# Optimization experiments

Measured on AMD Instinct MI355X. Metric: run time of the kernel, lower is better.

## Reference

```python
import jax, jax.numpy as jnp
import numpy as np

BLOCK_H = 1
BLOCK_W = 1
EPS = 1e-6


def setup_inputs() -> dict:
    key = jax.random.key(0)
    ks = jax.random.split(key, 8)
    B, L, D = 2, 4096, 1024
    NBF, DK = 16, 64  # nb_features, d_k (d_model // n_heads)
    ws = 1.0 / np.sqrt(D)  # nn.Linear-like init scale
    return {
        "q": jax.random.normal(ks[0], (B, L, D), jnp.float32),
        "k": jax.random.normal(ks[1], (B, L, D), jnp.float32),
        "v": jax.random.normal(ks[2], (B, L, D), jnp.float32),
        "w_q": jax.random.normal(ks[3], (D, D), jnp.float32) * ws,
        "w_k": jax.random.normal(ks[4], (D, D), jnp.float32) * ws,
        "w_v": jax.random.normal(ks[5], (D, D), jnp.float32) * ws,
        "w_o": jax.random.normal(ks[6], (D, D), jnp.float32) * ws,
        "omega": jax.random.normal(ks[7], (NBF, DK), jnp.float32) / np.sqrt(DK),
    }


def reference(q, k, v, w_q, w_k, w_v, w_o, omega):
    B, Lq, D = q.shape
    Lk = k.shape[1]
    NBF, DK = omega.shape
    H = D // DK

    # projections (torch nn.Linear: x @ W.T), split into heads
    qh = (q @ w_q.T).reshape(B, Lq, H, DK)
    kh = (k @ w_k.T).reshape(B, Lk, H, DK)
    vh = (v @ w_v.T).reshape(B, Lk, H, DK)

    qp = jnp.exp(-0.5 * jnp.square(jnp.einsum('blhd,fd->blhf', qh, omega)))
    kp = jnp.exp(-0.5 * jnp.square(jnp.einsum('blhd,fd->blhf', kh, omega)))
    qp = qp / (qp.sum(-1, keepdims=True) + EPS)
    kp = kp / (kp.sum(-1, keepdims=True) + EPS)

    # causal prefix sums over key positions
    K_cum = jnp.cumsum(kp, axis=1)                                    # [B,Lk,H,F]
    KV_cum = jnp.cumsum(kp[..., None] * vh[..., None, :], axis=1)     # [B,Lk,H,F,DK]

    # blockwise causal key index per query position
    q_idx = jnp.arange(Lq)
    key_idx = jnp.clip((q_idx // BLOCK_H + 1) * BLOCK_W - 1, 0, Lk - 1)
    K_sel = K_cum[:, key_idx]      # [B,Lq,H,F]
    KV_sel = KV_cum[:, key_idx]    # [B,Lq,H,F,DK]

    numerator = jnp.einsum('blhf,blhfd->blhd', qp, KV_sel)
    denominator = jnp.sum(qp * K_sel, axis=-1, keepdims=True)
    out = (numerator / (denominator + EPS)).reshape(B, Lq, D)
    return out @ w_o.T
```

## Files before the change

### kernel.cpp

```cpp
#include <hip/hip_runtime.h>

#define L_SEQ   4096
#define BATCH   2
#define DMODEL  1024
#define HEADS   16
#define DKH     64
#define NBF     16
#define CHUNK   64
#define NCHUNK  64
#define NCHAIN  32
#define STATE_SZ 1040
#define EPSF    1e-6f

typedef __attribute__((ext_vector_type(8))) __bf16 bf16x8;
typedef __attribute__((ext_vector_type(4))) float  floatx4;

__device__ __forceinline__ unsigned short f2bf(float x) {
  unsigned u = __builtin_bit_cast(unsigned, x);
  u += 0x7fffu + ((u >> 16) & 1u);
  return (unsigned short)(u >> 16);
}
__device__ __forceinline__ float bf2f(unsigned short u) {
  return __builtin_bit_cast(float, ((unsigned)u) << 16);
}

#define GLOAD16(gp, lp) \
  __builtin_amdgcn_global_load_lds((const __attribute__((address_space(1))) void*)(gp), \
                                   (__attribute__((address_space(3))) void*)(lp), 16, 0, 0)
#define WAIT_V4L0()  asm volatile("s_waitcnt vmcnt(4) lgkmcnt(0)" ::: "memory")
#define WAIT_V0L0()  asm volatile("s_waitcnt vmcnt(0) lgkmcnt(0)" ::: "memory")
#define SBAR()       __builtin_amdgcn_s_barrier()
#define SCHED0()     __builtin_amdgcn_sched_barrier(0)

__global__ __launch_bounds__(256) void prep(const float* __restrict__ wv, const float* __restrict__ wo,
                                            const float* __restrict__ wq, const float* __restrict__ wk,
                                            const float* __restrict__ omega,
                                            unsigned short* __restrict__ wvb, unsigned short* __restrict__ wob,
                                            unsigned short* __restrict__ wtq, unsigned short* __restrict__ wtk) {
  __shared__ float ws[64 * 64];
  __shared__ float oms[NBF * 64];
  const int blk = blockIdx.x;
  const int tid = threadIdx.x;
  if (blk < 2048) {
    const float* in = (blk < 1024) ? wv : wo;
    unsigned short* out = (blk < 1024) ? wvb : wob;
    int i = (blk & 1023) * 256 + tid;
    float4 v4 = ((const float4*)in)[i];
    ushort4 o;
    o.x = f2bf(v4.x); o.y = f2bf(v4.y); o.z = f2bf(v4.z); o.w = f2bf(v4.w);
    ((ushort4*)out)[i] = o;
    return;
  }
  const int local = blk - 2048;
  const int z = local >> 8;
  const int h = (local & 255) >> 4;
  const int s = local & 15;
  const float* w = z ? wk : wq;
  unsigned short* wt = z ? wtk : wtq;
  for (int i = tid; i < 64 * 64; i += 256) {
    int r = i >> 6, c = i & 63;
    ws[i] = w[(size_t)(h * 64 + r) * DMODEL + s * 64 + c];
  }
  for (int i = tid; i < NBF * 64; i += 256) oms[i] = omega[i];
  __syncthreads();
  for (int j = tid; j < NBF * 64; j += 256) {
    int f = j >> 6, c = j & 63;
    float acc = 0.f;
#pragma unroll
    for (int d = 0; d < 64; ++d) acc += oms[f * 64 + d] * ws[d * 64 + c];
    wt[(size_t)(h * NBF + f) * DMODEL + s * 64 + c] = f2bf(acc);
  }
}

__global__ __launch_bounds__(256) void proj_all(const float* __restrict__ q, const float* __restrict__ k,
                                                const float* __restrict__ v,
                                                const unsigned short* __restrict__ wtq,
                                                const unsigned short* __restrict__ wtk,
                                                const unsigned short* __restrict__ wvb,
                                                float* __restrict__ qp_t, float* __restrict__ kp_t,
                                                unsigned short* __restrict__ vh) {
  constexpr int K = DMODEL, NT = K / 32;
  __shared__ unsigned short As[2][128 * 32];
  __shared__ unsigned short Bs[2][128 * 32];
  const int tid  = threadIdx.x;
  const int wave = tid >> 6, lane = tid & 63;

  const int bid = blockIdx.x;
  const int id = (bid & 7) * 96 + (bid >> 3);
  int op, mt, nt;
  const float* A;
  const unsigned short* Bt;
  if (id < 256) {
    op = id >> 7;
    const int local = id & 127;
    nt = (local & 1) << 7;
    mt = (local >> 1) << 7;
    A  = op ? k : q;
    Bt = op ? wtk : wtq;
  } else {
    op = 2;
    const int local = id - 256;
    nt = (local & 7) << 7;
    mt = (local >> 3) << 7;
    A  = v;
    Bt = wvb;
  }

  const int wm = (wave >> 1) << 6, wn = (wave & 1) << 6;
  const int r16 = lane & 15, kg = lane >> 4;

  floatx4 acc[4][4];
#pragma unroll
  for (int m = 0; m < 4; ++m)
#pragma unroll
    for (int n = 0; n < 4; ++n) acc[m][n] = floatx4{0.f, 0.f, 0.f, 0.f};

  const int ar0  = tid >> 3;
  const int acol = (tid & 7) << 2;
  const float* aG = A + (size_t)(mt + ar0) * K + acol;
  const int ldrow = wave * 16 + (lane >> 2);
  const int ldcol = (lane & 3) << 3;
  const unsigned short* bG = Bt + (size_t)(nt + ldrow) * K + ldcol;

  float4 rA0[4], rA1[4];

  auto loadA = [&](float4* r, int kt) {
#pragma unroll
    for (int j = 0; j < 4; ++j) r[j] = *(const float4*)(aG + (size_t)32 * j * K + kt);
  };
  auto stageB = [&](int buf, int kt) {
    char* bL = (char*)Bs[buf] + wave * 1024;
    GLOAD16(bG + kt, bL);
    GLOAD16(bG + (size_t)64 * K + kt, bL + 4096);
  };
  auto writeA = [&](int buf, const float4* r) {
#pragma unroll
    for (int j = 0; j < 4; ++j) {
      ushort4 u;
      u.x = f2bf(r[j].x); u.y = f2bf(r[j].y); u.z = f2bf(r[j].z); u.w = f2bf(r[j].w);
      *(ushort4*)&As[buf][(ar0 + 32 * j) * 32 + acol] = u;
    }
  };
  auto mfmaStep = [&](int buf) {
    bf16x8 af[4], bfr[4];
#pragma unroll
    for (int m = 0; m < 4; ++m)
      af[m] = *(const bf16x8*)&As[buf][(wm + m * 16 + r16) * 32 + kg * 8];
#pragma unroll
    for (int n = 0; n < 4; ++n)
      bfr[n] = *(const bf16x8*)&Bs[buf][(wn + n * 16 + r16) * 32 + kg * 8];
#pragma unroll
    for (int m = 0; m < 4; ++m)
#pragma unroll
      for (int n = 0; n < 4; ++n)
        acc[m][n] = __builtin_amdgcn_mfma_f32_16x16x32_bf16(af[m], bfr[n], acc[m][n], 0, 0, 0);
  };

  loadA(rA0, 0);
  stageB(0, 0);
  SCHED0();
  writeA(0, rA0);
  loadA(rA1, 32);
  WAIT_V4L0();
  SCHED0();
  SBAR();

  for (int t = 0; t < NT; t += 2) {
    if (t + 1 < NT) stageB(1, (t + 1) * 32);
    SCHED0();
    if (t + 1 < NT) writeA(1, rA1);
    if (t + 2 < NT) loadA(rA0, (t + 2) * 32);
    mfmaStep(0);
    WAIT_V4L0();
    SCHED0();
    SBAR();
    if (t + 2 < NT) stageB(0, (t + 2) * 32);
    SCHED0();
    if (t + 2 < NT) writeA(0, rA0);
    if (t + 3 < NT) loadA(rA1, (t + 3) * 32);
    mfmaStep(1);
    WAIT_V4L0();
    SCHED0();
    SBAR();
  }

  if (op < 2) {
    float* xp_t = op ? kp_t : qp_t;
    const int hbase = (nt + wn) >> 4;
#pragma unroll
    for (int m = 0; m < 4; ++m) {
#pragma unroll
      for (int n = 0; n < 4; ++n) {
        const int hglob = hbase + n;
#pragma unroll
        for (int r = 0; r < 4; ++r) {
          float x = acc[m][n][r];
          float p = __expf(-0.5f * x * x);
          float s = p;
          s += __shfl_xor(s, 1);
          s += __shfl_xor(s, 2);
          s += __shfl_xor(s, 4);
          s += __shfl_xor(s, 8);
          float o = p / (s + EPSF);
          const int row = mt + wm + m * 16 + kg * 4 + r;
          const int b = row >> 12, l = row & 4095;
          xp_t[(((size_t)(b * HEADS + hglob)) * L_SEQ + l) * NBF + r16] = o;
        }
      }
    }
  } else {
#pragma unroll
    for (int m = 0; m < 4; ++m) {
      const int row0 = mt + wm + m * 16 + kg * 4;
#pragma unroll
      for (int n = 0; n < 4; ++n) {
        const int col = nt + wn + n * 16 + r16;
#pragma unroll
        for (int r = 0; r < 4; ++r)
          vh[(size_t)(row0 + r) * DMODEL + col] = f2bf(acc[m][n][r]);
      }
    }
  }
}

__global__ __launch_bounds__(256) void gemm_o(const unsigned short* __restrict__ A,
                                              const unsigned short* __restrict__ Bt,
                                              float* __restrict__ C) {
  constexpr int K = DMODEL, NT = K / 32;
  __shared__ unsigned short As[2][128 * 32];
  __shared__ unsigned short Bs[2][128 * 32];
  const int tid  = threadIdx.x;
  const int wave = tid >> 6, lane = tid & 63;
  const int bid = blockIdx.x;
  const int id = (bid & 7) * 64 + (bid >> 3);
  const int nt = (id & 7) << 7, mt = (id >> 3) << 7;
  const int wm = (wave >> 1) << 6, wn = (wave & 1) << 6;
  const int r16 = lane & 15, kg = lane >> 4;

  floatx4 acc[4][4];
#pragma unroll
  for (int m = 0; m < 4; ++m)
#pragma unroll
    for (int n = 0; n < 4; ++n) acc[m][n] = floatx4{0.f, 0.f, 0.f, 0.f};

  const int ldrow = wave * 16 + (lane >> 2);
  const int ldcol = (lane & 3) << 3;
  const unsigned short* aG = A  + (size_t)(mt + ldrow) * K + ldcol;
  const unsigned short* bG = Bt + (size_t)(nt + ldrow) * K + ldcol;

  auto stage = [&](int buf, int kt) {
    char* aL = (char*)As[buf] + wave * 1024;
    char* bL = (char*)Bs[buf] + wave * 1024;
    GLOAD16(aG + kt, aL);
    GLOAD16(aG + (size_t)64 * K + kt, aL + 4096);
    GLOAD16(bG + kt, bL);
    GLOAD16(bG + (size_t)64 * K + kt, bL + 4096);
  };

  stage(0, 0);
  WAIT_V0L0();
  SCHED0();
  SBAR();
  for (int t = 0; t < NT; ++t) {
    if (t + 1 < NT) stage((t + 1) & 1, (t + 1) * 32);
    const int buf = t & 1;
    bf16x8 af[4], bfr[4];
#pragma unroll
    for (int m = 0; m < 4; ++m)
      af[m] = *(const bf16x8*)&As[buf][(wm + m * 16 + r16) * 32 + kg * 8];
#pragma unroll
    for (int n = 0; n < 4; ++n)
      bfr[n] = *(const bf16x8*)&Bs[buf][(wn + n * 16 + r16) * 32 + kg * 8];
#pragma unroll
    for (int m = 0; m < 4; ++m)
#pragma unroll
      for (int n = 0; n < 4; ++n)
        acc[m][n] = __builtin_amdgcn_mfma_f32_16x16x32_bf16(af[m], bfr[n], acc[m][n], 0, 0, 0);
    WAIT_V0L0();
    SCHED0();
    SBAR();
  }

#pragma unroll
  for (int m = 0; m < 4; ++m) {
    const int row0 = mt + wm + m * 16 + kg * 4;
#pragma unroll
    for (int n = 0; n < 4; ++n) {
      const int col = nt + wn + n * 16 + r16;
#pragma unroll
      for (int r = 0; r < 4; ++r)
        C[(size_t)(row0 + r) * DMODEL + col] = acc[m][n][r];
    }
  }
}

__global__ __launch_bounds__(64) void scan_chunk_sum(const float* __restrict__ kp_t,
                                                     const unsigned short* __restrict__ vh,
                                                     float* __restrict__ Sws) {
  const int c = blockIdx.x & (NCHUNK - 1);
  const int chain = blockIdx.x >> 6;
  const int b = chain >> 4, h = chain & 15;
  const int d = threadIdx.x;
  __shared__ float kp_s[CHUNK * NBF];
  const float* kpB = kp_t + ((size_t)chain * L_SEQ + c * CHUNK) * NBF;
  for (int i = 0; i < 16; ++i) kp_s[d + i * 64] = kpB[d + i * 64];
  __syncthreads();
  float S[NBF];
#pragma unroll
  for (int f = 0; f < NBF; ++f) S[f] = 0.f;
  const unsigned short* vB = vh + ((size_t)(b * L_SEQ + c * CHUNK)) * DMODEL + h * DKH + d;
  for (int l = 0; l < CHUNK; ++l) {
    float vv = bf2f(vB[(size_t)l * DMODEL]);
#pragma unroll
    for (int f = 0; f < NBF; ++f) S[f] += kp_s[l * NBF + f] * vv;
  }
  float* out = Sws + ((size_t)chain * NCHUNK + c) * STATE_SZ;
#pragma unroll
  for (int f = 0; f < NBF; ++f) out[f * 64 + d] = S[f];
  if (d < NBF) {
    float ks = 0.f;
    for (int l = 0; l < CHUNK; ++l) ks += kp_s[l * NBF + d];
    out[1024 + d] = ks;
  }
}

__global__ __launch_bounds__(64) void scan_chunks(float* __restrict__ Sws) {
  const int chain = blockIdx.x;
  const int e = blockIdx.y * 64 + threadIdx.x;
  if (e >= STATE_SZ) return;
  float acc = 0.f;
  float* p = Sws + (size_t)chain * NCHUNK * STATE_SZ + e;
  for (int c = 0; c < NCHUNK; ++c) {
    float v = p[(size_t)c * STATE_SZ];
    p[(size_t)c * STATE_SZ] = acc;
    acc += v;
  }
}

__global__ __launch_bounds__(64) void scan_apply(const float* __restrict__ qp_t,
                                                 const float* __restrict__ kp_t,
                                                 const unsigned short* __restrict__ vh,
                                                 const float* __restrict__ Sws,
                                                 unsigned short* __restrict__ attn) {
  const int c = blockIdx.x & (NCHUNK - 1);
  const int chain = blockIdx.x >> 6;
  const int b = chain >> 4, h = chain & 15;
  const int d = threadIdx.x;
  __shared__ float kp_s[CHUNK * NBF];
  __shared__ float qp_s[CHUNK * NBF];
  {
    const float* kpB = kp_t + ((size_t)chain * L_SEQ + c * CHUNK) * NBF;
    const float* qpB = qp_t + ((size_t)chain * L_SEQ + c * CHUNK) * NBF;
    for (int i = 0; i < 16; ++i) {
      kp_s[d + i * 64] = kpB[d + i * 64];
      qp_s[d + i * 64] = qpB[d + i * 64];
    }
  }
  __syncthreads();
  const float* st = Sws + ((size_t)chain * NCHUNK + c) * STATE_SZ;
  float S[NBF], kc[NBF];
#pragma unroll
  for (int f = 0; f < NBF; ++f) S[f] = st[f * 64 + d];
#pragma unroll
  for (int f = 0; f < NBF; ++f) kc[f] = st[1024 + f];
  const unsigned short* vB = vh + ((size_t)(b * L_SEQ + c * CHUNK)) * DMODEL + h * DKH + d;
  unsigned short* oB = attn + ((size_t)(b * L_SEQ + c * CHUNK)) * DMODEL + h * DKH + d;
  for (int l = 0; l < CHUNK; ++l) {
    float vv = bf2f(vB[(size_t)l * DMODEL]);
    float num = 0.f, den = 0.f;
#pragma unroll
    for (int f = 0; f < NBF; ++f) {
      float kpf = kp_s[l * NBF + f];
      S[f]  += kpf * vv;
      kc[f] += kpf;
      float qpf = qp_s[l * NBF + f];
      num += qpf * S[f];
      den += qpf * kc[f];
    }
    oB[(size_t)l * DMODEL] = f2bf(num / (den + EPSF));
  }
}

extern "C" void kernel_launch(void* const* d_in, const int* in_sizes, int n_in,
                              void* d_out, int out_size, void* d_ws, size_t ws_size,
                              hipStream_t stream) {
  const float* q   = (const float*)d_in[0];
  const float* k   = (const float*)d_in[1];
  const float* v   = (const float*)d_in[2];
  const float* w_q = (const float*)d_in[3];
  const float* w_k = (const float*)d_in[4];
  const float* w_v = (const float*)d_in[5];
  const float* w_o = (const float*)d_in[6];
  const float* omega = (const float*)d_in[7];
  float* out = (float*)d_out;

  constexpr size_t NQ = (size_t)BATCH * L_SEQ * DMODEL;
  constexpr size_t NW = (size_t)DMODEL * DMODEL;
  constexpr size_t NWT = (size_t)HEADS * NBF * DMODEL;
  constexpr size_t NP = (size_t)BATCH * HEADS * L_SEQ * NBF;
  constexpr size_t NS = (size_t)NCHAIN * NCHUNK * STATE_SZ;

  char* ws = (char*)d_ws;
  size_t off = 0;
  auto alc = [&](size_t bytes) { void* p = ws + off; off += (bytes + 255) & ~(size_t)255; return p; };
  unsigned short* wvb = (unsigned short*)alc(NW * 2);
  unsigned short* wob = (unsigned short*)alc(NW * 2);
  unsigned short* wtq = (unsigned short*)alc(NWT * 2);
  unsigned short* wtk = (unsigned short*)alc(NWT * 2);
  unsigned short* vh  = (unsigned short*)alc(NQ * 2);
  unsigned short* attn = (unsigned short*)alc(NQ * 2);
  float* qp  = (float*)alc(NP * 4);
  float* kp  = (float*)alc(NP * 4);
  float* Sws = (float*)alc(NS * 4);

  prep<<<2560, 256, 0, stream>>>(w_v, w_o, w_q, w_k, omega, wvb, wob, wtq, wtk);
  proj_all<<<768, 256, 0, stream>>>(q, k, v, wtq, wtk, wvb, qp, kp, vh);

  scan_chunk_sum<<<NCHAIN * NCHUNK, 64, 0, stream>>>(kp, vh, Sws);
  scan_chunks<<<dim3(NCHAIN, (STATE_SZ + 63) / 64), 64, 0, stream>>>(Sws);
  scan_apply<<<NCHAIN * NCHUNK, 64, 0, stream>>>(qp, kp, vh, Sws, attn);

  gemm_o<<<512, 256, 0, stream>>>(attn, wob, out);
}
```

Before: 169.6 us.

## Swizzle LDS tiles, stage fp32 A via direct loads, drop double buffering

Both GEMM kernels switch to single-buffered LDS tiles with XOR-swizzled column placement, aiming to reduce LDS bank conflicts on the fragment reads. In proj_all the fp32 activations are now copied straight into LDS with global_load_lds and converted to bf16 at fragment-read time, removing the register staging and the convert-then-store path. The hand-tuned double-buffered pipeline with explicit waitcnt and barriers is replaced by a simple load, __syncthreads, compute, __syncthreads loop. This gives up overlap of global loads with MFMA work, which may expose memory latency.

```diff
diff --git a/kernel.cpp b/kernel.cpp
--- a/kernel.cpp
+++ b/kernel.cpp
@@ -27,10 +27,6 @@
 #define GLOAD16(gp, lp) \
   __builtin_amdgcn_global_load_lds((const __attribute__((address_space(1))) void*)(gp), \
                                    (__attribute__((address_space(3))) void*)(lp), 16, 0, 0)
-#define WAIT_V4L0()  asm volatile("s_waitcnt vmcnt(4) lgkmcnt(0)" ::: "memory")
-#define WAIT_V0L0()  asm volatile("s_waitcnt vmcnt(0) lgkmcnt(0)" ::: "memory")
-#define SBAR()       __builtin_amdgcn_s_barrier()
-#define SCHED0()     __builtin_amdgcn_sched_barrier(0)
 
 __global__ __launch_bounds__(256) void prep(const float* __restrict__ wv, const float* __restrict__ wo,
                                             const float* __restrict__ wq, const float* __restrict__ wk,
@@ -79,9 +75,11 @@
                                                 const unsigned short* __restrict__ wvb,
                                                 float* __restrict__ qp_t, float* __restrict__ kp_t,
                                                 unsigned short* __restrict__ vh) {
-  constexpr int K = DMODEL, NT = K / 32;
-  __shared__ unsigned short As[2][128 * 32];
-  __shared__ unsigned short Bs[2][128 * 32];
+  constexpr int K = DMODEL;
+  __shared__ char smem[24576];
+  float* As = (float*)smem;
+  unsigned short* Bs = (unsigned short*)(smem + 16384);
+
   const int tid  = threadIdx.x;
   const int wave = tid >> 6, lane = tid & 63;
 
@@ -115,73 +113,46 @@
 #pragma unroll
     for (int n = 0; n < 4; ++n) acc[m][n] = floatx4{0.f, 0.f, 0.f, 0.f};
 
-  const int ar0  = tid >> 3;
-  const int acol = (tid & 7) << 2;
-  const float* aG = A + (size_t)(mt + ar0) * K + acol;
-  const int ldrow = wave * 16 + (lane >> 2);
-  const int ldcol = (lane & 3) << 3;
-  const unsigned short* bG = Bt + (size_t)(nt + ldrow) * K + ldcol;
-
-  float4 rA0[4], rA1[4];
-
-  auto loadA = [&](float4* r, int kt) {
-#pragma unroll
-    for (int j = 0; j < 4; ++j) r[j] = *(const float4*)(aG + (size_t)32 * j * K + kt);
-  };
-  auto stageB = [&](int buf, int kt) {
-    char* bL = (char*)Bs[buf] + wave * 1024;
-    GLOAD16(bG + kt, bL);
-    GLOAD16(bG + (size_t)64 * K + kt, bL + 4096);
-  };
-  auto writeA = [&](int buf, const float4* r) {
-#pragma unroll
-    for (int j = 0; j < 4; ++j) {
-      ushort4 u;
-      u.x = f2bf(r[j].x); u.y = f2bf(r[j].y); u.z = f2bf(r[j].z); u.w = f2bf(r[j].w);
-      *(ushort4*)&As[buf][(ar0 + 32 * j) * 32 + acol] = u;
-    }
-  };
-  auto mfmaStep = [&](int buf) {
+  const int arow = wave * 32 + (lane >> 3);
+  const int acolsw = ((lane & 7) ^ (lane >> 3)) << 2;
+  const float* aG = A + (size_t)(mt + arow) * K + acolsw;
+  const int brow = wave * 16 + (lane >> 2);
+  const int bcolsw = (((lane & 3) ^ ((lane >> 3) & 3)) << 3);
+  const unsigned short* bG = Bt + (size_t)(nt + brow) * K + bcolsw;
+
+  for (int kt = 0; kt < K; kt += 32) {
+#pragma unroll
+    for (int j = 0; j < 4; ++j)
+      GLOAD16(aG + (size_t)(8 * j) * K + kt, smem + wave * 4096 + j * 1024);
+    GLOAD16(bG + kt, (char*)Bs + wave * 1024);
+    GLOAD16(bG + (size_t)64 * K + kt, (char*)Bs + 4096 + wave * 1024);
+    __syncthreads();
+
     bf16x8 af[4], bfr[4];
 #pragma unroll
-    for (int m = 0; m < 4; ++m)
-      af[m] = *(const bf16x8*)&As[buf][(wm + m * 16 + r16) * 32 + kg * 8];
-#pragma unroll
-    for (int n = 0; n < 4; ++n)
-      bfr[n] = *(const bf16x8*)&Bs[buf][(wn + n * 16 + r16) * 32 + kg * 8];
+    for (int m = 0; m < 4; ++m) {
+      const int row = wm + m * 16 + r16;
+      const int sA = (kg << 1) ^ (r16 & 7);
+      floatx4 lo = *(const floatx4*)(smem + row * 128 + sA * 16);
+      floatx4 hi = *(const floatx4*)(smem + row * 128 + (sA ^ 1) * 16);
+#pragma unroll
+      for (int t2 = 0; t2 < 4; ++t2) {
+        af[m][t2]     = (__bf16)lo[t2];
+        af[m][4 + t2] = (__bf16)hi[t2];
+      }
+    }
+#pragma unroll
+    for (int n = 0; n < 4; ++n) {
+      const int row = wn + n * 16 + r16;
+      const int sB = kg ^ ((r16 >> 1) & 3);
+      bfr[n] = *(const bf16x8*)((char*)Bs + row * 64 + sB * 16);
+    }
 #pragma unroll
     for (int m = 0; m < 4; ++m)
 #pragma unroll
       for (int n = 0; n < 4; ++n)
         acc[m][n] = __builtin_amdgcn_mfma_f32_16x16x32_bf16(af[m], bfr[n], acc[m][n], 0, 0, 0);
-  };
-
-  loadA(rA0, 0);
-  stageB(0, 0);
-  SCHED0();
-  writeA(0, rA0);
-  loadA(rA1, 32);
-  WAIT_V4L0();
-  SCHED0();
-  SBAR();
-
-  for (int t = 0; t < NT; t += 2) {
-    if (t + 1 < NT) stageB(1, (t + 1) * 32);
-    SCHED0();
-    if (t + 1 < NT) writeA(1, rA1);
-    if (t + 2 < NT) loadA(rA0, (t + 2) * 32);
-    mfmaStep(0);
-    WAIT_V4L0();
-    SCHED0();
-    SBAR();
-    if (t + 2 < NT) stageB(0, (t + 2) * 32);
-    SCHED0();
-    if (t + 2 < NT) writeA(0, rA0);
-    if (t + 3 < NT) loadA(rA1, (t + 3) * 32);
-    mfmaStep(1);
-    WAIT_V4L0();
-    SCHED0();
-    SBAR();
+    __syncthreads();
   }
 
   if (op < 2) {
@@ -226,9 +197,9 @@
 __global__ __launch_bounds__(256) void gemm_o(const unsigned short* __restrict__ A,
                                               const unsigned short* __restrict__ Bt,
                                               float* __restrict__ C) {
-  constexpr int K = DMODEL, NT = K / 32;
-  __shared__ unsigned short As[2][128 * 32];
-  __shared__ unsigned short Bs[2][128 * 32];
+  constexpr int K = DMODEL;
+  __shared__ unsigned short As[128 * 32];
+  __shared__ unsigned short Bs[128 * 32];
   const int tid  = threadIdx.x;
   const int wave = tid >> 6, lane = tid & 63;
   const int bid = blockIdx.x;
@@ -244,41 +215,36 @@
     for (int n = 0; n < 4; ++n) acc[m][n] = floatx4{0.f, 0.f, 0.f, 0.f};
 
   const int ldrow = wave * 16 + (lane >> 2);
-  const int ldcol = (lane & 3) << 3;
-  const unsigned short* aG = A  + (size_t)(mt + ldrow) * K + ldcol;
-  const unsigned short* bG = Bt + (size_t)(nt + ldrow) * K + ldcol;
-
-  auto stage = [&](int buf, int kt) {
-    char* aL = (char*)As[buf] + wave * 1024;
-    char* bL = (char*)Bs[buf] + wave * 1024;
-    GLOAD16(aG + kt, aL);
-    GLOAD16(aG + (size_t)64 * K + kt, aL + 4096);
-    GLOAD16(bG + kt, bL);
-    GLOAD16(bG + (size_t)64 * K + kt, bL + 4096);
-  };
-
-  stage(0, 0);
-  WAIT_V0L0();
-  SCHED0();
-  SBAR();
-  for (int t = 0; t < NT; ++t) {
-    if (t + 1 < NT) stage((t + 1) & 1, (t + 1) * 32);
-    const int buf = t & 1;
+  const int ldcolsw = (((lane & 3) ^ ((lane >> 3) & 3)) << 3);
+  const unsigned short* aG = A  + (size_t)(mt + ldrow) * K + ldcolsw;
+  const unsigned short* bG = Bt + (size_t)(nt + ldrow) * K + ldcolsw;
+
+  for (int kt = 0; kt < K; kt += 32) {
+    GLOAD16(aG + kt, (char*)As + wave * 1024);
+    GLOAD16(aG + (size_t)64 * K + kt, (char*)As + 4096 + wave * 1024);
+    GLOAD16(bG + kt, (char*)Bs + wave * 1024);
+    GLOAD16(bG + (size_t)64 * K + kt, (char*)Bs + 4096 + wave * 1024);
+    __syncthreads();
+
     bf16x8 af[4], bfr[4];
 #pragma unroll
-    for (int m = 0; m < 4; ++m)
-      af[m] = *(const bf16x8*)&As[buf][(wm + m * 16 + r16) * 32 + kg * 8];
-#pragma unroll
-    for (int n = 0; n < 4; ++n)
-      bfr[n] = *(const bf16x8*)&Bs[buf][(wn + n * 16 + r16) * 32 + kg * 8];
+    for (int m = 0; m < 4; ++m) {
+      const int row = wm + m * 16 + r16;
+      const int sA = kg ^ ((r16 >> 1) & 3);
+      af[m] = *(const bf16x8*)((char*)As + row * 64 + sA * 16);
+    }
+#pragma unroll
+    for (int n = 0; n < 4; ++n) {
+      const int row = wn + n * 16 + r16;
+      const int sB = kg ^ ((r16 >> 1) & 3);
+      bfr[n] = *(const bf16x8*)((char*)Bs + row * 64 + sB * 16);
+    }
 #pragma unroll
     for (int m = 0; m < 4; ++m)
 #pragma unroll
       for (int n = 0; n < 4; ++n)
         acc[m][n] = __builtin_amdgcn_mfma_f32_16x16x32_bf16(af[m], bfr[n], acc[m][n], 0, 0, 0);
-    WAIT_V0L0();
-    SCHED0();
-    SBAR();
+    __syncthreads();
   }
 
 #pragma unroll
```

Result: no change. 167.5 us (-1.2%).
